# Performance work log

Measured on AMD Instinct MI355X. Metric: run time of the kernel, lower is better.

Reference implementation:

```python
import jax, jax.numpy as jnp
import numpy as np

U = 100000   # user_count
I = 50000    # item_count
N = U + I    # total nodes in bipartite graph
D = 64       # embedding dim
L = 3        # num_layers
E = 4800000  # nnz of normalized adjacency
B = 8192     # batch size


def setup_inputs() -> dict:
    key = jax.random.key(0)
    ks = jax.random.split(key, 8)
    edge_src = jax.random.randint(ks[0], (E,), 0, N, dtype=jnp.int32)
    edge_dst = jax.random.randint(ks[1], (E,), 0, N, dtype=jnp.int32)
    # normalized adjacency values ~ 1/sqrt(deg_i*deg_j); small positive numbers
    edge_val = jax.random.uniform(ks[2], (E,), dtype=jnp.float32) * (1.0 / 32.0)
    user_emb_w = jax.random.normal(ks[3], (U, D), dtype=jnp.float32) * 0.01
    item_emb_w = jax.random.normal(ks[4], (I, D), dtype=jnp.float32) * 0.01
    batch_user = jax.random.randint(ks[5], (B,), 0, U, dtype=jnp.int32)
    batch_pos_item = jax.random.randint(ks[6], (B,), 0, I, dtype=jnp.int32)
    batch_neg_item = jax.random.randint(ks[7], (B,), 0, I, dtype=jnp.int32)
    return {
        "edge_src": edge_src,
        "edge_dst": edge_dst,
        "edge_val": edge_val,
        "user_emb_w": user_emb_w,
        "item_emb_w": item_emb_w,
        "batch_user": batch_user,
        "batch_pos_item": batch_pos_item,
        "batch_neg_item": batch_neg_item,
    }


def _spmm(edge_src, edge_dst, edge_val, x):
    # out[i] = sum_{e: dst[e]==i} val[e] * x[src[e]]  (sparse A @ x)
    msgs = edge_val[:, None] * x[edge_src]           # [E, D]
    return jax.ops.segment_sum(msgs, edge_dst, num_segments=N)


def _computer(edge_src, edge_dst, edge_val, user_emb_w, item_emb_w):
    all_emb = jnp.concatenate([user_emb_w, item_emb_w], axis=0)  # [N, D]
    acc = all_emb
    cur = all_emb
    for _ in range(L):
        cur = _spmm(edge_src, edge_dst, edge_val, cur)
        acc = acc + cur
    light_out = acc / jnp.float32(L + 1)  # mean over (L+1) layer embeddings
    return light_out[:U], light_out[U:]


def reference(edge_src, edge_dst, edge_val, user_emb_w, item_emb_w,
              batch_user, batch_pos_item, batch_neg_item):
    all_users, all_items = _computer(edge_src, edge_dst, edge_val,
                                     user_emb_w, item_emb_w)
    user = all_users[batch_user]       # [B, D]
    pos = all_items[batch_pos_item]    # [B, D]
    neg = all_items[batch_neg_item]    # [B, D]
    pos_score = jnp.sum(user * pos, axis=1)
    neg_score = jnp.sum(user * neg, axis=1)
    user0 = user_emb_w[batch_user]
    pos0 = item_emb_w[batch_pos_item]
    neg0 = item_emb_w[batch_neg_item]
    reg_loss = (jnp.sum(user0 * user0) + jnp.sum(pos0 * pos0)
                + jnp.sum(neg0 * neg0))
    return pos_score, neg_score, reg_loss
```

## Files before the change

### kernel.cpp

```cpp
#include <hip/hip_runtime.h>

#define D 64
#define BK 256
#define KMAX 1024
#define PCH 6144
#define PEPT 6

static __device__ __forceinline__ unsigned short f2bf(float f) {
    unsigned int u = __float_as_uint(f);
    unsigned int r = (u + 0x7FFFu + ((u >> 16) & 1u)) >> 16;
    return (unsigned short)r;
}
static __device__ __forceinline__ float bflo(unsigned int u) {
    return __uint_as_float(u << 16);
}
static __device__ __forceinline__ float bfhi(unsigned int u) {
    return __uint_as_float(u & 0xFFFF0000u);
}

__global__ void init_kernel(const float4* __restrict__ user_w,
                            const float4* __restrict__ item_w,
                            float4* __restrict__ acc,
                            ushort4* __restrict__ curb,
                            const int* __restrict__ flags,
                            int n_user4, int n_tot4) {
    int i = blockIdx.x * blockDim.x + threadIdx.x;
    if (i >= n_tot4) return;
    float4 v = (i < n_user4) ? user_w[i] : item_w[i - n_user4];
    ushort4 b;
    b.x = f2bf(v.x); b.y = f2bf(v.y); b.z = f2bf(v.z); b.w = f2bf(v.w);
    curb[i] = b;
    if (flags[i >> 4]) acc[i] = v;
}

__global__ void flag_kernel(const int* __restrict__ bu,
                            const int* __restrict__ bp,
                            const int* __restrict__ bn,
                            int* __restrict__ flags,
                            int* __restrict__ list,
                            int* __restrict__ n_list,
                            int U_, int B_) {
    int t = blockIdx.x * blockDim.x + threadIdx.x;
    int node = -1;
    if (t < 3 * B_) {
        if (t < B_)            node = bu[t];
        else if (t < 2 * B_)   node = U_ + bp[t - B_];
        else                   node = U_ + bn[t - 2 * B_];
    }
    int old = 1;
    if (node >= 0) old = atomicExch(&flags[node], 1);
    unsigned long long m = __ballot(old == 0);
    int lane = threadIdx.x & 63;
    int myoff = __popcll(m & ((1ull << lane) - 1ull));
    int total = __popcll(m);
    int bse = 0;
    if (lane == 0 && total) bse = atomicAdd(n_list, total);
    bse = __shfl(bse, 0, 64);
    if (old == 0) list[bse + myoff] = node;
}

__global__ void __launch_bounds__(1024)
partition_kernel(const int* __restrict__ src,
                 const int* __restrict__ dst,
                 const float* __restrict__ val,
                 int* __restrict__ g_pos,
                 int2* __restrict__ st,
                 int S_, int K_, int E_) {
    __shared__ int2 stg[PCH];
    __shared__ int cnt[KMAX];
    __shared__ int sh[KMAX];
    __shared__ int gb[KMAX];
    int tid = threadIdx.x;
    for (int k = tid; k < K_; k += 1024) cnt[k] = 0;
    __syncthreads();
    int b0 = blockIdx.x * PCH;
    int nc = min(PCH, E_ - b0);
    int myk[PEPT], myr[PEPT], mysrc[PEPT];
    unsigned mypk[PEPT];
#pragma unroll
    for (int e = 0; e < PEPT; ++e) {
        int i = b0 + e * 1024 + tid;
        if (i < E_) {
            int d = dst[i];
            int k = d >> 8;
            myk[e] = k;
            mysrc[e] = src[i];
            mypk[e] = ((unsigned)f2bf(val[i]) << 16) | (unsigned)(d & (BK - 1));
            myr[e] = atomicAdd(&cnt[k], 1);
        } else {
            myk[e] = -1;
        }
    }
    __syncthreads();
    int v = (tid < K_) ? cnt[tid] : 0;
    sh[tid] = v;
    __syncthreads();
    for (int off = 1; off < KMAX; off <<= 1) {
        int t = (tid >= off) ? sh[tid - off] : 0;
        __syncthreads();
        sh[tid] += t;
        __syncthreads();
    }
    if (tid < K_ && v) {
        int lbase = sh[tid] - v;
        gb[tid] = (tid * S_ + atomicAdd(&g_pos[tid], v)) - lbase;
    }
    __syncthreads();
#pragma unroll
    for (int e = 0; e < PEPT; ++e) {
        int k = myk[e];
        if (k >= 0) {
            int slot = (sh[k] - cnt[k]) + myr[e];
            stg[slot] = make_int2(mysrc[e] | (k << 20), (int)mypk[e]);
        }
    }
    __syncthreads();
    for (int l = tid; l < nc; l += 1024) {
        int2 ev = stg[l];
        int k = (int)((unsigned)ev.x >> 20);
        st[gb[k] + l] = make_int2(ev.x & 0xFFFFF, ev.y);
    }
}

__global__ void scan_bkt_kernel(const int* __restrict__ cnt,
                                int* __restrict__ base, int K_) {
    __shared__ int sh[KMAX];
    int tid = threadIdx.x;
    int v = (tid < K_) ? cnt[tid] : 0;
    sh[tid] = v;
    __syncthreads();
    for (int off = 1; off < KMAX; off <<= 1) {
        int t = (tid >= off) ? sh[tid - off] : 0;
        __syncthreads();
        sh[tid] += t;
        __syncthreads();
    }
    if (tid < K_) base[tid] = sh[tid] - v;
}

__global__ void __launch_bounds__(1024)
place_kernel(const int2* __restrict__ st,
             const int* __restrict__ g_cnt,
             const int* __restrict__ bkt_base,
             int2* __restrict__ row_span,
             int2* __restrict__ col_val,
             int S_, int N_) {
    __shared__ int ldeg[BK];
    __shared__ int sh[BK];
    __shared__ int lcur[BK];
    int b = blockIdx.x;
    int tid = threadIdx.x;
    int rbeg = b << 8;
    int sbeg = b * S_;
    int cnt = g_cnt[b];
    int cbeg = bkt_base[b];
    if (tid < BK) ldeg[tid] = 0;
    __syncthreads();
    for (int i = tid; i < cnt; i += 1024)
        atomicAdd(&ldeg[(unsigned)st[sbeg + i].y & (BK - 1u)], 1);
    __syncthreads();
    int v = 0;
    if (tid < BK) {
        v = ldeg[tid];
        sh[tid] = v;
    }
    __syncthreads();
    for (int off = 1; off < BK; off <<= 1) {
        int t = (tid < BK && tid >= off) ? sh[tid - off] : 0;
        __syncthreads();
        if (tid < BK) sh[tid] += t;
        __syncthreads();
    }
    if (tid < BK) {
        int excl = sh[tid] - v;
        lcur[tid] = excl;
        int gi = rbeg + tid;
        if (gi < N_) row_span[gi] = make_int2(cbeg + excl, cbeg + excl + v);
    }
    __syncthreads();
    for (int i = tid; i < cnt; i += 1024) {
        int2 cv = st[sbeg + i];
        int pcur = cbeg + atomicAdd(&lcur[(unsigned)cv.y & (BK - 1u)], 1);
        col_val[pcur] = cv;
    }
}

static __device__ __forceinline__ void spmm_row_body(
        int beg, int end, int lane, int q, int lid,
        const int2* __restrict__ col_val, const uint4* __restrict__ xb,
        float& s0, float& s1, float& s2, float& s3,
        float& s4, float& s5, float& s6, float& s7) {
    for (int base = beg; base < end; base += 64) {
        int e = base + lane;
        int c = 0;
        float v = 0.f;
        if (e < end) {
            int2 cv = col_val[e];
            c = cv.x;
            v = bfhi((unsigned)cv.y);
        }
        int nq = (min(64, end - base) + 7) >> 3;
        uint4 t0, t1, t2, t3, t4, t5, t6, t7;
        float w0, w1, w2, w3, w4, w5, w6, w7;
        { int cj = __shfl(c, q, 64);      w0 = __shfl(v, q, 64);      t0 = xb[cj * 8 + lid]; }
        if (nq > 1) { int cj = __shfl(c, 8 + q, 64);  w1 = __shfl(v, 8 + q, 64);  t1 = xb[cj * 8 + lid]; }
        if (nq > 2) { int cj = __shfl(c, 16 + q, 64); w2 = __shfl(v, 16 + q, 64); t2 = xb[cj * 8 + lid]; }
        if (nq > 3) { int cj = __shfl(c, 24 + q, 64); w3 = __shfl(v, 24 + q, 64); t3 = xb[cj * 8 + lid]; }
        if (nq > 4) { int cj = __shfl(c, 32 + q, 64); w4 = __shfl(v, 32 + q, 64); t4 = xb[cj * 8 + lid]; }
        if (nq > 5) { int cj = __shfl(c, 40 + q, 64); w5 = __shfl(v, 40 + q, 64); t5 = xb[cj * 8 + lid]; }
        if (nq > 6) { int cj = __shfl(c, 48 + q, 64); w6 = __shfl(v, 48 + q, 64); t6 = xb[cj * 8 + lid]; }
        if (nq > 7) { int cj = __shfl(c, 56 + q, 64); w7 = __shfl(v, 56 + q, 64); t7 = xb[cj * 8 + lid]; }
#define ACC8(W, T) \
        s0 += (W) * bflo((T).x); s1 += (W) * bfhi((T).x); \
        s2 += (W) * bflo((T).y); s3 += (W) * bfhi((T).y); \
        s4 += (W) * bflo((T).z); s5 += (W) * bfhi((T).z); \
        s6 += (W) * bflo((T).w); s7 += (W) * bfhi((T).w);
        { ACC8(w0, t0) }
        if (nq > 1) { ACC8(w1, t1) }
        if (nq > 2) { ACC8(w2, t2) }
        if (nq > 3) { ACC8(w3, t3) }
        if (nq > 4) { ACC8(w4, t4) }
        if (nq > 5) { ACC8(w5, t5) }
        if (nq > 6) { ACC8(w6, t6) }
        if (nq > 7) { ACC8(w7, t7) }
#undef ACC8
    }
#pragma unroll
    for (int off = 32; off >= 8; off >>= 1) {
        s0 += __shfl_xor(s0, off, 64);
        s1 += __shfl_xor(s1, off, 64);
        s2 += __shfl_xor(s2, off, 64);
        s3 += __shfl_xor(s3, off, 64);
        s4 += __shfl_xor(s4, off, 64);
        s5 += __shfl_xor(s5, off, 64);
        s6 += __shfl_xor(s6, off, 64);
        s7 += __shfl_xor(s7, off, 64);
    }
}

__global__ void spmm_csr_kernel(const int2* __restrict__ row_span,
                                const int2* __restrict__ col_val,
                                const uint4* __restrict__ xb,
                                uint4* __restrict__ nxtb,
                                float4* __restrict__ acc,
                                const int* __restrict__ flags,
                                int N_) {
    int row = (int)((blockIdx.x * blockDim.x + threadIdx.x) >> 6);
    int lane = threadIdx.x & 63;
    if (row >= N_) return;
    int q = lane >> 3;
    int lid = lane & 7;
    int2 sp = row_span[row];
    float s0 = 0, s1 = 0, s2 = 0, s3 = 0, s4 = 0, s5 = 0, s6 = 0, s7 = 0;
    spmm_row_body(sp.x, sp.y, lane, q, lid, col_val, xb,
                  s0, s1, s2, s3, s4, s5, s6, s7);
    if (q == 0) {
        uint4 b;
        b.x = (unsigned)f2bf(s0) | ((unsigned)f2bf(s1) << 16);
        b.y = (unsigned)f2bf(s2) | ((unsigned)f2bf(s3) << 16);
        b.z = (unsigned)f2bf(s4) | ((unsigned)f2bf(s5) << 16);
        b.w = (unsigned)f2bf(s6) | ((unsigned)f2bf(s7) << 16);
        nxtb[row * 8 + lid] = b;
        if (flags[row]) {
            float4* ap = acc + row * 16 + lid * 2;
            float4 a0 = ap[0];
            a0.x += s0; a0.y += s1; a0.z += s2; a0.w += s3;
            ap[0] = a0;
            float4 a1 = ap[1];
            a1.x += s4; a1.y += s5; a1.z += s6; a1.w += s7;
            ap[1] = a1;
        }
    }
}

__global__ void spmm_rows_kernel(const int2* __restrict__ row_span,
                                 const int2* __restrict__ col_val,
                                 const uint4* __restrict__ xb,
                                 float4* __restrict__ acc,
                                 const int* __restrict__ list,
                                 const int* __restrict__ n_list) {
    int w = (int)((blockIdx.x * blockDim.x + threadIdx.x) >> 6);
    if (w >= *n_list) return;
    int row = list[w];
    int lane = threadIdx.x & 63;
    int q = lane >> 3;
    int lid = lane & 7;
    int2 sp = row_span[row];
    float s0 = 0, s1 = 0, s2 = 0, s3 = 0, s4 = 0, s5 = 0, s6 = 0, s7 = 0;
    spmm_row_body(sp.x, sp.y, lane, q, lid, col_val, xb,
                  s0, s1, s2, s3, s4, s5, s6, s7);
    if (q == 0) {
        float4* ap = acc + row * 16 + lid * 2;
        float4 a0 = ap[0];
        a0.x += s0; a0.y += s1; a0.z += s2; a0.w += s3;
        ap[0] = a0;
        float4 a1 = ap[1];
        a1.x += s4; a1.y += s5; a1.z += s6; a1.w += s7;
        ap[1] = a1;
    }
}

__global__ void final_kernel(const float* __restrict__ acc,
                             const float* __restrict__ user_w,
                             const float* __restrict__ item_w,
                             const int* __restrict__ bu,
                             const int* __restrict__ bp,
                             const int* __restrict__ bn,
                             float* __restrict__ out,
                             float* __restrict__ red,
                             int U_, int B_) {
    __shared__ float pr[4];
    int w = (int)((blockIdx.x * blockDim.x + threadIdx.x) >> 6);
    int lane = threadIdx.x & 63;
    bool valid = (w < B_);
    float ps = 0.f, ns = 0.f, r = 0.f;
    if (valid) {
        int iu = bu[w], ip = bp[w], in_ = bn[w];
        const float scale = 0.25f;
        float u = acc[(long)iu * D + lane] * scale;
        float p = acc[(long)(U_ + ip) * D + lane] * scale;
        float g = acc[(long)(U_ + in_) * D + lane] * scale;
        ps = u * p;
        ns = u * g;
        float u0 = user_w[(long)iu * D + lane];
        float p0 = item_w[(long)ip * D + lane];
        float n0 = item_w[(long)in_ * D + lane];
        r = u0 * u0 + p0 * p0 + n0 * n0;
    }
#pragma unroll
    for (int off = 32; off; off >>= 1) {
        ps += __shfl_down(ps, off, 64);
        ns += __shfl_down(ns, off, 64);
        r  += __shfl_down(r, off, 64);
    }
    if (lane == 0) pr[threadIdx.x >> 6] = r;
    __syncthreads();
    if (threadIdx.x == 0)
        red[blockIdx.x] = pr[0] + pr[1] + pr[2] + pr[3];
    if (valid && lane == 0) {
        out[w] = ps;
        out[B_ + w] = ns;
    }
}

__global__ void reduce_kernel(const float* __restrict__ red,
                              float* __restrict__ out_scalar, int nblk) {
    __shared__ float sh[256];
    float s = 0.f;
    for (int i = threadIdx.x; i < nblk; i += 256) s += red[i];
    sh[threadIdx.x] = s;
    __syncthreads();
    for (int off = 128; off; off >>= 1) {
        if (threadIdx.x < off) sh[threadIdx.x] += sh[threadIdx.x + off];
        __syncthreads();
    }
    if (threadIdx.x == 0) *out_scalar = sh[0];
}

extern "C" void kernel_launch(void* const* d_in, const int* in_sizes, int n_in,
                              void* d_out, int out_size, void* d_ws, size_t ws_size,
                              hipStream_t stream) {
    const int*   edge_src = (const int*)d_in[0];
    const int*   edge_dst = (const int*)d_in[1];
    const float* edge_val = (const float*)d_in[2];
    const float* user_w   = (const float*)d_in[3];
    const float* item_w   = (const float*)d_in[4];
    const int*   bu       = (const int*)d_in[5];
    const int*   bp       = (const int*)d_in[6];
    const int*   bn       = (const int*)d_in[7];

    int E_ = in_sizes[0];
    int U_ = in_sizes[3] / D;
    int I_ = in_sizes[4] / D;
    int B_ = in_sizes[5];
    int N_ = U_ + I_;
    long ND = (long)N_ * D;
    int K_ = (N_ + BK - 1) >> 8;
    int S_ = ((E_ / K_) * 3 / 2 + 255) & ~255;

    char* p = (char*)d_ws;
    int2* col_val  = (int2*)p;   p += (size_t)E_ * sizeof(int2);
    int2* row_span = (int2*)p;   p += (size_t)N_ * sizeof(int2);
    int*  bkt_base = (int*)p;    p += KMAX * sizeof(int);
    float* red     = (float*)p;  p += 4096 * sizeof(float);
    char* zb = p;
    int*  g_pos    = (int*)p;    p += KMAX * sizeof(int);
    int*  n_list   = (int*)p;    p += 256;
    int*  flags    = (int*)p;    p += (size_t)N_ * sizeof(int);
    size_t zbytes  = (size_t)(p - zb);
    int*  list     = (int*)p;    p += (size_t)3 * B_ * sizeof(int);
    p = (char*)(((uintptr_t)p + 255) & ~(uintptr_t)255);
    int2* st = (int2*)p;
    float* acc = (float*)p;
    unsigned short* curb = (unsigned short*)(acc + ND);
    unsigned short* nxtb = curb + ND;
    float* out = (float*)d_out;

    int n4 = (int)(ND / 4);
    int nu4 = U_ * D / 4;

    hipMemsetAsync(zb, 0, zbytes, stream);
    partition_kernel<<<(E_ + PCH - 1) / PCH, 1024, 0, stream>>>(
        edge_src, edge_dst, edge_val, g_pos, st, S_, K_, E_);
    scan_bkt_kernel<<<1, KMAX, 0, stream>>>(g_pos, bkt_base, K_);
    place_kernel<<<K_, 1024, 0, stream>>>(st, g_pos, bkt_base, row_span,
                                          col_val, S_, N_);

    flag_kernel<<<(3 * B_ + 255) / 256, 256, 0, stream>>>(
        bu, bp, bn, flags, list, n_list, U_, B_);

    init_kernel<<<(n4 + 255) / 256, 256, 0, stream>>>(
        (const float4*)user_w, (const float4*)item_w,
        (float4*)acc, (ushort4*)curb, flags, nu4, n4);

    spmm_csr_kernel<<<(N_ + 3) / 4, 256, 0, stream>>>(
        row_span, col_val, (const uint4*)curb, (uint4*)nxtb, (float4*)acc,
        flags, N_);
    spmm_csr_kernel<<<(N_ + 3) / 4, 256, 0, stream>>>(
        row_span, col_val, (const uint4*)nxtb, (uint4*)curb, (float4*)acc,
        flags, N_);
    spmm_rows_kernel<<<(3 * B_ + 3) / 4, 256, 0, stream>>>(
        row_span, col_val, (const uint4*)curb, (float4*)acc, list, n_list);

    int nblk = (B_ * 64 + 255) / 256;
    final_kernel<<<nblk, 256, 0, stream>>>(
        acc, user_w, item_w, bu, bp, bn, out, red, U_, B_);
    reduce_kernel<<<1, 256, 0, stream>>>(red, out + 2 * B_, nblk);
}
```

Baseline: 402.4 us.

## Persistent SpMM with next-row prefetch, fold bucket scan into place kernel

The CSR SpMM kernel becomes a grid-stride persistent kernel with a fixed grid. Each wave prefetches the next row's span and first col/val chunk while it finishes the current row, hiding index-load latency. The separate single-block bucket scan is removed: every place block redundantly scans the bucket counts in shared memory, saving a launch at the cost of extra per-block work. place_kernel also keeps up to 8 staged edges in registers between the histogram and scatter passes so they are not reloaded.

```diff
diff --git a/kernel.cpp b/kernel.cpp
--- a/kernel.cpp
+++ b/kernel.cpp
@@ -122,29 +122,13 @@
     }
 }
 
-__global__ void scan_bkt_kernel(const int* __restrict__ cnt,
-                                int* __restrict__ base, int K_) {
-    __shared__ int sh[KMAX];
-    int tid = threadIdx.x;
-    int v = (tid < K_) ? cnt[tid] : 0;
-    sh[tid] = v;
-    __syncthreads();
-    for (int off = 1; off < KMAX; off <<= 1) {
-        int t = (tid >= off) ? sh[tid - off] : 0;
-        __syncthreads();
-        sh[tid] += t;
-        __syncthreads();
-    }
-    if (tid < K_) base[tid] = sh[tid] - v;
-}
-
 __global__ void __launch_bounds__(1024)
 place_kernel(const int2* __restrict__ st,
-             const int* __restrict__ g_cnt,
-             const int* __restrict__ bkt_base,
+             const int* __restrict__ g_pos,
              int2* __restrict__ row_span,
              int2* __restrict__ col_val,
-             int S_, int N_) {
+             int S_, int K_, int N_) {
+    __shared__ int gsc[KMAX];
     __shared__ int ldeg[BK];
     __shared__ int sh[BK];
     __shared__ int lcur[BK];
@@ -152,11 +136,26 @@
     int tid = threadIdx.x;
     int rbeg = b << 8;
     int sbeg = b * S_;
-    int cnt = g_cnt[b];
-    int cbeg = bkt_base[b];
+    int gp = (tid < K_) ? g_pos[tid] : 0;
+    gsc[tid] = gp;
     if (tid < BK) ldeg[tid] = 0;
     __syncthreads();
-    for (int i = tid; i < cnt; i += 1024)
+    for (int off = 1; off < KMAX; off <<= 1) {
+        int t = (tid >= off) ? gsc[tid - off] : 0;
+        __syncthreads();
+        gsc[tid] += t;
+        __syncthreads();
+    }
+    int cbeg = (b > 0) ? gsc[b - 1] : 0;
+    int cnt = gsc[b] - cbeg;
+    int2 ec0, ec1, ec2, ec3, ec4, ec5, ec6, ec7;
+#define HLOAD(J, EC) { int i = tid + (J) * 1024; \
+        EC = (i < cnt) ? st[sbeg + i] : make_int2(0, 0); \
+        if (i < cnt) atomicAdd(&ldeg[(unsigned)EC.y & (BK - 1u)], 1); }
+    HLOAD(0, ec0) HLOAD(1, ec1) HLOAD(2, ec2) HLOAD(3, ec3)
+    HLOAD(4, ec4) HLOAD(5, ec5) HLOAD(6, ec6) HLOAD(7, ec7)
+#undef HLOAD
+    for (int i = tid + 8192; i < cnt; i += 1024)
         atomicAdd(&ldeg[(unsigned)st[sbeg + i].y & (BK - 1u)], 1);
     __syncthreads();
     int v = 0;
@@ -178,10 +177,17 @@
         if (gi < N_) row_span[gi] = make_int2(cbeg + excl, cbeg + excl + v);
     }
     __syncthreads();
-    for (int i = tid; i < cnt; i += 1024) {
+#define SCAT(J, EC) { int i = tid + (J) * 1024; \
+        if (i < cnt) { \
+            int p = cbeg + atomicAdd(&lcur[(unsigned)EC.y & (BK - 1u)], 1); \
+            col_val[p] = EC; } }
+    SCAT(0, ec0) SCAT(1, ec1) SCAT(2, ec2) SCAT(3, ec3)
+    SCAT(4, ec4) SCAT(5, ec5) SCAT(6, ec6) SCAT(7, ec7)
+#undef SCAT
+    for (int i = tid + 8192; i < cnt; i += 1024) {
         int2 cv = st[sbeg + i];
-        int pcur = cbeg + atomicAdd(&lcur[(unsigned)cv.y & (BK - 1u)], 1);
-        col_val[pcur] = cv;
+        int p = cbeg + atomicAdd(&lcur[(unsigned)cv.y & (BK - 1u)], 1);
+        col_val[p] = cv;
     }
 }
 
@@ -238,30 +244,123 @@
     }
 }
 
-__global__ void spmm_csr_kernel(const int2* __restrict__ row_span,
-                                const int2* __restrict__ col_val,
-                                const uint4* __restrict__ xb,
-                                uint4* __restrict__ nxtb,
-                                float4* __restrict__ acc,
-                                const int* __restrict__ flags,
-                                int N_) {
-    int row = (int)((blockIdx.x * blockDim.x + threadIdx.x) >> 6);
+__global__ void __launch_bounds__(256)
+spmm_csr_kernel(const int2* __restrict__ row_span,
+                const int2* __restrict__ col_val,
+                const uint4* __restrict__ xb,
+                uint4* __restrict__ nxtb,
+                float4* __restrict__ acc,
+                const int* __restrict__ flags,
+                int N_) {
     int lane = threadIdx.x & 63;
-    if (row >= N_) return;
     int q = lane >> 3;
     int lid = lane & 7;
+    int nw = (int)((gridDim.x * blockDim.x) >> 6);
+    int row = (int)((blockIdx.x * blockDim.x + threadIdx.x) >> 6);
+    if (row >= N_) return;
     int2 sp = row_span[row];
-    float s0 = 0, s1 = 0, s2 = 0, s3 = 0, s4 = 0, s5 = 0, s6 = 0, s7 = 0;
-    spmm_row_body(sp.x, sp.y, lane, q, lid, col_val, xb,
-                  s0, s1, s2, s3, s4, s5, s6, s7);
-    if (q == 0) {
-        uint4 b;
-        b.x = (unsigned)f2bf(s0) | ((unsigned)f2bf(s1) << 16);
-        b.y = (unsigned)f2bf(s2) | ((unsigned)f2bf(s3) << 16);
-        b.z = (unsigned)f2bf(s4) | ((unsigned)f2bf(s5) << 16);
-        b.w = (unsigned)f2bf(s6) | ((unsigned)f2bf(s7) << 16);
-        nxtb[row * 8 + lid] = b;
-        if (flags[row]) {
+    int2 cv = make_int2(0, 0);
+    if (sp.x + lane < sp.y) cv = col_val[sp.x + lane];
+    while (true) {
+        int nrow = row + nw;
+        int2 spn = make_int2(0, 0);
+        if (nrow < N_) spn = row_span[nrow];
+        float s0 = 0, s1 = 0, s2 = 0, s3 = 0, s4 = 0, s5 = 0, s6 = 0, s7 = 0;
+        int base = sp.x;
+        int end = sp.y;
+        int c = cv.x;
+        float v = bfhi((unsigned)cv.y);
+        if (base < end) {
+            while (true) {
+                int nq = (min(64, end - base) + 7) >> 3;
+                uint4 t0, t1, t2, t3, t4, t5, t6, t7;
+                float w0, w1, w2, w3, w4, w5, w6, w7;
+                { int cj = __shfl(c, q, 64);      w0 = __shfl(v, q, 64);      t0 = xb[cj * 8 + lid]; }
+                if (nq > 1) { int cj = __shfl(c, 8 + q, 64);  w1 = __shfl(v, 8 + q, 64);  t1 = xb[cj * 8 + lid]; }
+                if (nq > 2) { int cj = __shfl(c, 16 + q, 64); w2 = __shfl(v, 16 + q, 64); t2 = xb[cj * 8 + lid]; }
+                if (nq > 3) { int cj = __shfl(c, 24 + q, 64); w3 = __shfl(v, 24 + q, 64); t3 = xb[cj * 8 + lid]; }
+                if (nq > 4) { int cj = __shfl(c, 32 + q, 64); w4 = __shfl(v, 32 + q, 64); t4 = xb[cj * 8 + lid]; }
+                if (nq > 5) { int cj = __shfl(c, 40 + q, 64); w5 = __shfl(v, 40 + q, 64); t5 = xb[cj * 8 + lid]; }
+                if (nq > 6) { int cj = __shfl(c, 48 + q, 64); w6 = __shfl(v, 48 + q, 64); t6 = xb[cj * 8 + lid]; }
+                if (nq > 7) { int cj = __shfl(c, 56 + q, 64); w7 = __shfl(v, 56 + q, 64); t7 = xb[cj * 8 + lid]; }
+#define ACC8(W, T) \
+                s0 += (W) * bflo((T).x); s1 += (W) * bfhi((T).x); \
+                s2 += (W) * bflo((T).y); s3 += (W) * bfhi((T).y); \
+                s4 += (W) * bflo((T).z); s5 += (W) * bfhi((T).z); \
+                s6 += (W) * bflo((T).w); s7 += (W) * bfhi((T).w);
+                { ACC8(w0, t0) }
+                if (nq > 1) { ACC8(w1, t1) }
+                if (nq > 2) { ACC8(w2, t2) }
+                if (nq > 3) { ACC8(w3, t3) }
+                if (nq > 4) { ACC8(w4, t4) }
+                if (nq > 5) { ACC8(w5, t5) }
+                if (nq > 6) { ACC8(w6, t6) }
+                if (nq > 7) { ACC8(w7, t7) }
+#undef ACC8
+                base += 64;
+                if (base >= end) break;
+                int e = base + lane;
+                int2 cvi = (e < end) ? col_val[e] : make_int2(0, 0);
+                c = cvi.x;
+                v = bfhi((unsigned)cvi.y);
+            }
+        }
+        int2 cvn = make_int2(0, 0);
+        if (nrow < N_ && spn.x + lane < spn.y) cvn = col_val[spn.x + lane];
+#pragma unroll
+        for (int off = 32; off >= 8; off >>= 1) {
+            s0 += __shfl_xor(s0, off, 64);
+            s1 += __shfl_xor(s1, off, 64);
+            s2 += __shfl_xor(s2, off, 64);
+            s3 += __shfl_xor(s3, off, 64);
+            s4 += __shfl_xor(s4, off, 64);
+            s5 += __shfl_xor(s5, off, 64);
+            s6 += __shfl_xor(s6, off, 64);
+            s7 += __shfl_xor(s7, off, 64);
+        }
+        if (q == 0) {
+            uint4 b;
+            b.x = (unsigned)f2bf(s0) | ((unsigned)f2bf(s1) << 16);
+            b.y = (unsigned)f2bf(s2) | ((unsigned)f2bf(s3) << 16);
+            b.z = (unsigned)f2bf(s4) | ((unsigned)f2bf(s5) << 16);
+            b.w = (unsigned)f2bf(s6) | ((unsigned)f2bf(s7) << 16);
+            nxtb[row * 8 + lid] = b;
+            if (flags[row]) {
+                float4* ap = acc + row * 16 + lid * 2;
+                float4 a0 = ap[0];
+                a0.x += s0; a0.y += s1; a0.z += s2; a0.w += s3;
+                ap[0] = a0;
+                float4 a1 = ap[1];
+                a1.x += s4; a1.y += s5; a1.z += s6; a1.w += s7;
+                ap[1] = a1;
+            }
+        }
+        if (nrow >= N_) break;
+        row = nrow;
+        sp = spn;
+        cv = cvn;
+    }
+}
+
+__global__ void spmm_rows_kernel(const int2* __restrict__ row_span,
+                                 const int2* __restrict__ col_val,
+                                 const uint4* __restrict__ xb,
+                                 float4* __restrict__ acc,
+                                 const int* __restrict__ list,
+                                 const int* __restrict__ n_list) {
+    int lane = threadIdx.x & 63;
+    int q = lane >> 3;
+    int lid = lane & 7;
+    int nw = (int)((gridDim.x * blockDim.x) >> 6);
+    int nl = *n_list;
+    for (int w = (int)((blockIdx.x * blockDim.x + threadIdx.x) >> 6); w < nl;
+         w += nw) {
+        int row = list[w];
+        int2 sp = row_span[row];
+        float s0 = 0, s1 = 0, s2 = 0, s3 = 0, s4 = 0, s5 = 0, s6 = 0, s7 = 0;
+        spmm_row_body(sp.x, sp.y, lane, q, lid, col_val, xb,
+                      s0, s1, s2, s3, s4, s5, s6, s7);
+        if (q == 0) {
             float4* ap = acc + row * 16 + lid * 2;
             float4 a0 = ap[0];
             a0.x += s0; a0.y += s1; a0.z += s2; a0.w += s3;
@@ -270,33 +369,6 @@
             a1.x += s4; a1.y += s5; a1.z += s6; a1.w += s7;
             ap[1] = a1;
         }
-    }
-}
-
-__global__ void spmm_rows_kernel(const int2* __restrict__ row_span,
-                                 const int2* __restrict__ col_val,
-                                 const uint4* __restrict__ xb,
-                                 float4* __restrict__ acc,
-                                 const int* __restrict__ list,
-                                 const int* __restrict__ n_list) {
-    int w = (int)((blockIdx.x * blockDim.x + threadIdx.x) >> 6);
-    if (w >= *n_list) return;
-    int row = list[w];
-    int lane = threadIdx.x & 63;
-    int q = lane >> 3;
-    int lid = lane & 7;
-    int2 sp = row_span[row];
-    float s0 = 0, s1 = 0, s2 = 0, s3 = 0, s4 = 0, s5 = 0, s6 = 0, s7 = 0;
-    spmm_row_body(sp.x, sp.y, lane, q, lid, col_val, xb,
-                  s0, s1, s2, s3, s4, s5, s6, s7);
-    if (q == 0) {
-        float4* ap = acc + row * 16 + lid * 2;
-        float4 a0 = ap[0];
-        a0.x += s0; a0.y += s1; a0.z += s2; a0.w += s3;
-        ap[0] = a0;
-        float4 a1 = ap[1];
-        a1.x += s4; a1.y += s5; a1.z += s6; a1.w += s7;
-        ap[1] = a1;
     }
 }
 
@@ -381,7 +453,6 @@
     char* p = (char*)d_ws;
     int2* col_val  = (int2*)p;   p += (size_t)E_ * sizeof(int2);
     int2* row_span = (int2*)p;   p += (size_t)N_ * sizeof(int2);
-    int*  bkt_base = (int*)p;    p += KMAX * sizeof(int);
     float* red     = (float*)p;  p += 4096 * sizeof(float);
     char* zb = p;
     int*  g_pos    = (int*)p;    p += KMAX * sizeof(int);
@@ -402,9 +473,8 @@
     hipMemsetAsync(zb, 0, zbytes, stream);
     partition_kernel<<<(E_ + PCH - 1) / PCH, 1024, 0, stream>>>(
         edge_src, edge_dst, edge_val, g_pos, st, S_, K_, E_);
-    scan_bkt_kernel<<<1, KMAX, 0, stream>>>(g_pos, bkt_base, K_);
-    place_kernel<<<K_, 1024, 0, stream>>>(st, g_pos, bkt_base, row_span,
-                                          col_val, S_, N_);
+    place_kernel<<<K_, 1024, 0, stream>>>(st, g_pos, row_span, col_val,
+                                          S_, K_, N_);
 
     flag_kernel<<<(3 * B_ + 255) / 256, 256, 0, stream>>>(
         bu, bp, bn, flags, list, n_list, U_, B_);
@@ -413,13 +483,13 @@
         (const float4*)user_w, (const float4*)item_w,
         (float4*)acc, (ushort4*)curb, flags, nu4, n4);
 
-    spmm_csr_kernel<<<(N_ + 3) / 4, 256, 0, stream>>>(
+    spmm_csr_kernel<<<2048, 256, 0, stream>>>(
         row_span, col_val, (const uint4*)curb, (uint4*)nxtb, (float4*)acc,
         flags, N_);
-    spmm_csr_kernel<<<(N_ + 3) / 4, 256, 0, stream>>>(
+    spmm_csr_kernel<<<2048, 256, 0, stream>>>(
         row_span, col_val, (const uint4*)nxtb, (uint4*)curb, (float4*)acc,
         flags, N_);
-    spmm_rows_kernel<<<(3 * B_ + 3) / 4, 256, 0, stream>>>(
+    spmm_rows_kernel<<<512, 256, 0, stream>>>(
         row_span, col_val, (const uint4*)curb, (float4*)acc, list, n_list);
 
     int nblk = (B_ * 64 + 255) / 256;
```

Result: slower. 434.1 us (+7.9%).

## Fold bucket scan into place kernel, register-cache edges, nontemporal CSR loads

Applied to the files above, without the earlier changes.

Removes the separate single-block scan launch by having each place_kernel block redundantly scan the bucket counts in shared memory. place_kernel now keeps up to eight edges per thread in registers between the histogram and scatter passes instead of reading the staging buffer twice. The SpMM kernels read col_val and row_span with nontemporal loads so the streamed CSR data does not evict the gathered embedding rows from cache. The redundant scan adds per-block work and barriers, and the register caching raises register pressure in a 1024-thread block.

```diff
diff --git a/kernel.cpp b/kernel.cpp
--- a/kernel.cpp
+++ b/kernel.cpp
@@ -16,6 +16,13 @@
 }
 static __device__ __forceinline__ float bfhi(unsigned int u) {
     return __uint_as_float(u & 0xFFFF0000u);
+}
+static __device__ __forceinline__ int2 nt_load_i2(const int2* p) {
+    long long t = __builtin_nontemporal_load((const long long*)p);
+    int2 r;
+    r.x = (int)(unsigned)(t & 0xFFFFFFFFull);
+    r.y = (int)(unsigned)((unsigned long long)t >> 32);
+    return r;
 }
 
 __global__ void init_kernel(const float4* __restrict__ user_w,
@@ -122,29 +129,13 @@
     }
 }
 
-__global__ void scan_bkt_kernel(const int* __restrict__ cnt,
-                                int* __restrict__ base, int K_) {
-    __shared__ int sh[KMAX];
-    int tid = threadIdx.x;
-    int v = (tid < K_) ? cnt[tid] : 0;
-    sh[tid] = v;
-    __syncthreads();
-    for (int off = 1; off < KMAX; off <<= 1) {
-        int t = (tid >= off) ? sh[tid - off] : 0;
-        __syncthreads();
-        sh[tid] += t;
-        __syncthreads();
-    }
-    if (tid < K_) base[tid] = sh[tid] - v;
-}
-
 __global__ void __launch_bounds__(1024)
 place_kernel(const int2* __restrict__ st,
-             const int* __restrict__ g_cnt,
-             const int* __restrict__ bkt_base,
+             const int* __restrict__ g_pos,
              int2* __restrict__ row_span,
              int2* __restrict__ col_val,
-             int S_, int N_) {
+             int S_, int K_, int N_) {
+    __shared__ int gsc[KMAX];
     __shared__ int ldeg[BK];
     __shared__ int sh[BK];
     __shared__ int lcur[BK];
@@ -152,11 +143,26 @@
     int tid = threadIdx.x;
     int rbeg = b << 8;
     int sbeg = b * S_;
-    int cnt = g_cnt[b];
-    int cbeg = bkt_base[b];
+    int gp = (tid < K_) ? g_pos[tid] : 0;
+    gsc[tid] = gp;
     if (tid < BK) ldeg[tid] = 0;
     __syncthreads();
-    for (int i = tid; i < cnt; i += 1024)
+    for (int off = 1; off < KMAX; off <<= 1) {
+        int t = (tid >= off) ? gsc[tid - off] : 0;
+        __syncthreads();
+        gsc[tid] += t;
+        __syncthreads();
+    }
+    int cbeg = (b > 0) ? gsc[b - 1] : 0;
+    int cnt = gsc[b] - cbeg;
+    int2 ec0, ec1, ec2, ec3, ec4, ec5, ec6, ec7;
+#define HLOAD(J, EC) { int i = tid + (J) * 1024; \
+        EC = (i < cnt) ? st[sbeg + i] : make_int2(0, 0); \
+        if (i < cnt) atomicAdd(&ldeg[(unsigned)EC.y & (BK - 1u)], 1); }
+    HLOAD(0, ec0) HLOAD(1, ec1) HLOAD(2, ec2) HLOAD(3, ec3)
+    HLOAD(4, ec4) HLOAD(5, ec5) HLOAD(6, ec6) HLOAD(7, ec7)
+#undef HLOAD
+    for (int i = tid + 8192; i < cnt; i += 1024)
         atomicAdd(&ldeg[(unsigned)st[sbeg + i].y & (BK - 1u)], 1);
     __syncthreads();
     int v = 0;
@@ -178,10 +184,17 @@
         if (gi < N_) row_span[gi] = make_int2(cbeg + excl, cbeg + excl + v);
     }
     __syncthreads();
-    for (int i = tid; i < cnt; i += 1024) {
+#define SCAT(J, EC) { int i = tid + (J) * 1024; \
+        if (i < cnt) { \
+            int p = cbeg + atomicAdd(&lcur[(unsigned)EC.y & (BK - 1u)], 1); \
+            col_val[p] = EC; } }
+    SCAT(0, ec0) SCAT(1, ec1) SCAT(2, ec2) SCAT(3, ec3)
+    SCAT(4, ec4) SCAT(5, ec5) SCAT(6, ec6) SCAT(7, ec7)
+#undef SCAT
+    for (int i = tid + 8192; i < cnt; i += 1024) {
         int2 cv = st[sbeg + i];
-        int pcur = cbeg + atomicAdd(&lcur[(unsigned)cv.y & (BK - 1u)], 1);
-        col_val[pcur] = cv;
+        int p = cbeg + atomicAdd(&lcur[(unsigned)cv.y & (BK - 1u)], 1);
+        col_val[p] = cv;
     }
 }
 
@@ -195,7 +208,7 @@
         int c = 0;
         float v = 0.f;
         if (e < end) {
-            int2 cv = col_val[e];
+            int2 cv = nt_load_i2(&col_val[e]);
             c = cv.x;
             v = bfhi((unsigned)cv.y);
         }
@@ -250,7 +263,7 @@
     if (row >= N_) return;
     int q = lane >> 3;
     int lid = lane & 7;
-    int2 sp = row_span[row];
+    int2 sp = nt_load_i2(&row_span[row]);
     float s0 = 0, s1 = 0, s2 = 0, s3 = 0, s4 = 0, s5 = 0, s6 = 0, s7 = 0;
     spmm_row_body(sp.x, sp.y, lane, q, lid, col_val, xb,
                   s0, s1, s2, s3, s4, s5, s6, s7);
@@ -381,7 +394,6 @@
     char* p = (char*)d_ws;
     int2* col_val  = (int2*)p;   p += (size_t)E_ * sizeof(int2);
     int2* row_span = (int2*)p;   p += (size_t)N_ * sizeof(int2);
-    int*  bkt_base = (int*)p;    p += KMAX * sizeof(int);
     float* red     = (float*)p;  p += 4096 * sizeof(float);
     char* zb = p;
     int*  g_pos    = (int*)p;    p += KMAX * sizeof(int);
@@ -402,9 +414,8 @@
     hipMemsetAsync(zb, 0, zbytes, stream);
     partition_kernel<<<(E_ + PCH - 1) / PCH, 1024, 0, stream>>>(
         edge_src, edge_dst, edge_val, g_pos, st, S_, K_, E_);
-    scan_bkt_kernel<<<1, KMAX, 0, stream>>>(g_pos, bkt_base, K_);
-    place_kernel<<<K_, 1024, 0, stream>>>(st, g_pos, bkt_base, row_span,
-                                          col_val, S_, N_);
+    place_kernel<<<K_, 1024, 0, stream>>>(st, g_pos, row_span, col_val,
+                                          S_, K_, N_);
 
     flag_kernel<<<(3 * B_ + 255) / 256, 256, 0, stream>>>(
         bu, bp, bn, flags, list, n_list, U_, B_);
```

New measurement: 396.6 us. Within noise of the previous version (-1.5%).

## Fuse graph prep kernels and build CSR in place with first SpMM layer

Applied to the files above, without the earlier changes.

Merges partition, bf16 conversion of the embeddings and batch flagging into one multi-role prep kernel. The bucket-scan and separate CSR placement pass are dropped: each bucket sorts its edges in place inside a fixed-size slot and immediately computes the first SpMM layer from them, reading the reordered edges through coherent atomic loads. The layer-0 embedding add moves into the final kernel, so acc no longer needs to be initialised. This removes several launches and one full edge-array copy, but fixed slots of 9216 per bucket silently truncate buckets with more edges, and the per-bucket SpMM uses only 16 wavefronts per 256 rows.

```diff
diff --git a/kernel.cpp b/kernel.cpp
--- a/kernel.cpp
+++ b/kernel.cpp
@@ -5,6 +5,8 @@
 #define KMAX 1024
 #define PCH 6144
 #define PEPT 6
+#define SLOT 9216
+#define NSL 9
 
 static __device__ __forceinline__ unsigned short f2bf(float f) {
     unsigned int u = __float_as_uint(f);
@@ -17,177 +19,19 @@
 static __device__ __forceinline__ float bfhi(unsigned int u) {
     return __uint_as_float(u & 0xFFFF0000u);
 }
-
-__global__ void init_kernel(const float4* __restrict__ user_w,
-                            const float4* __restrict__ item_w,
-                            float4* __restrict__ acc,
-                            ushort4* __restrict__ curb,
-                            const int* __restrict__ flags,
-                            int n_user4, int n_tot4) {
-    int i = blockIdx.x * blockDim.x + threadIdx.x;
-    if (i >= n_tot4) return;
-    float4 v = (i < n_user4) ? user_w[i] : item_w[i - n_user4];
-    ushort4 b;
-    b.x = f2bf(v.x); b.y = f2bf(v.y); b.z = f2bf(v.z); b.w = f2bf(v.w);
-    curb[i] = b;
-    if (flags[i >> 4]) acc[i] = v;
-}
-
-__global__ void flag_kernel(const int* __restrict__ bu,
-                            const int* __restrict__ bp,
-                            const int* __restrict__ bn,
-                            int* __restrict__ flags,
-                            int* __restrict__ list,
-                            int* __restrict__ n_list,
-                            int U_, int B_) {
-    int t = blockIdx.x * blockDim.x + threadIdx.x;
-    int node = -1;
-    if (t < 3 * B_) {
-        if (t < B_)            node = bu[t];
-        else if (t < 2 * B_)   node = U_ + bp[t - B_];
-        else                   node = U_ + bn[t - 2 * B_];
-    }
-    int old = 1;
-    if (node >= 0) old = atomicExch(&flags[node], 1);
-    unsigned long long m = __ballot(old == 0);
-    int lane = threadIdx.x & 63;
-    int myoff = __popcll(m & ((1ull << lane) - 1ull));
-    int total = __popcll(m);
-    int bse = 0;
-    if (lane == 0 && total) bse = atomicAdd(n_list, total);
-    bse = __shfl(bse, 0, 64);
-    if (old == 0) list[bse + myoff] = node;
-}
-
-__global__ void __launch_bounds__(1024)
-partition_kernel(const int* __restrict__ src,
-                 const int* __restrict__ dst,
-                 const float* __restrict__ val,
-                 int* __restrict__ g_pos,
-                 int2* __restrict__ st,
-                 int S_, int K_, int E_) {
-    __shared__ int2 stg[PCH];
-    __shared__ int cnt[KMAX];
-    __shared__ int sh[KMAX];
-    __shared__ int gb[KMAX];
-    int tid = threadIdx.x;
-    for (int k = tid; k < K_; k += 1024) cnt[k] = 0;
-    __syncthreads();
-    int b0 = blockIdx.x * PCH;
-    int nc = min(PCH, E_ - b0);
-    int myk[PEPT], myr[PEPT], mysrc[PEPT];
-    unsigned mypk[PEPT];
-#pragma unroll
-    for (int e = 0; e < PEPT; ++e) {
-        int i = b0 + e * 1024 + tid;
-        if (i < E_) {
-            int d = dst[i];
-            int k = d >> 8;
-            myk[e] = k;
-            mysrc[e] = src[i];
-            mypk[e] = ((unsigned)f2bf(val[i]) << 16) | (unsigned)(d & (BK - 1));
-            myr[e] = atomicAdd(&cnt[k], 1);
-        } else {
-            myk[e] = -1;
-        }
-    }
-    __syncthreads();
-    int v = (tid < K_) ? cnt[tid] : 0;
-    sh[tid] = v;
-    __syncthreads();
-    for (int off = 1; off < KMAX; off <<= 1) {
-        int t = (tid >= off) ? sh[tid - off] : 0;
-        __syncthreads();
-        sh[tid] += t;
-        __syncthreads();
-    }
-    if (tid < K_ && v) {
-        int lbase = sh[tid] - v;
-        gb[tid] = (tid * S_ + atomicAdd(&g_pos[tid], v)) - lbase;
-    }
-    __syncthreads();
-#pragma unroll
-    for (int e = 0; e < PEPT; ++e) {
-        int k = myk[e];
-        if (k >= 0) {
-            int slot = (sh[k] - cnt[k]) + myr[e];
-            stg[slot] = make_int2(mysrc[e] | (k << 20), (int)mypk[e]);
-        }
-    }
-    __syncthreads();
-    for (int l = tid; l < nc; l += 1024) {
-        int2 ev = stg[l];
-        int k = (int)((unsigned)ev.x >> 20);
-        st[gb[k] + l] = make_int2(ev.x & 0xFFFFF, ev.y);
-    }
-}
-
-__global__ void scan_bkt_kernel(const int* __restrict__ cnt,
-                                int* __restrict__ base, int K_) {
-    __shared__ int sh[KMAX];
-    int tid = threadIdx.x;
-    int v = (tid < K_) ? cnt[tid] : 0;
-    sh[tid] = v;
-    __syncthreads();
-    for (int off = 1; off < KMAX; off <<= 1) {
-        int t = (tid >= off) ? sh[tid - off] : 0;
-        __syncthreads();
-        sh[tid] += t;
-        __syncthreads();
-    }
-    if (tid < K_) base[tid] = sh[tid] - v;
-}
-
-__global__ void __launch_bounds__(1024)
-place_kernel(const int2* __restrict__ st,
-             const int* __restrict__ g_cnt,
-             const int* __restrict__ bkt_base,
-             int2* __restrict__ row_span,
-             int2* __restrict__ col_val,
-             int S_, int N_) {
-    __shared__ int ldeg[BK];
-    __shared__ int sh[BK];
-    __shared__ int lcur[BK];
-    int b = blockIdx.x;
-    int tid = threadIdx.x;
-    int rbeg = b << 8;
-    int sbeg = b * S_;
-    int cnt = g_cnt[b];
-    int cbeg = bkt_base[b];
-    if (tid < BK) ldeg[tid] = 0;
-    __syncthreads();
-    for (int i = tid; i < cnt; i += 1024)
-        atomicAdd(&ldeg[(unsigned)st[sbeg + i].y & (BK - 1u)], 1);
-    __syncthreads();
-    int v = 0;
-    if (tid < BK) {
-        v = ldeg[tid];
-        sh[tid] = v;
-    }
-    __syncthreads();
-    for (int off = 1; off < BK; off <<= 1) {
-        int t = (tid < BK && tid >= off) ? sh[tid - off] : 0;
-        __syncthreads();
-        if (tid < BK) sh[tid] += t;
-        __syncthreads();
-    }
-    if (tid < BK) {
-        int excl = sh[tid] - v;
-        lcur[tid] = excl;
-        int gi = rbeg + tid;
-        if (gi < N_) row_span[gi] = make_int2(cbeg + excl, cbeg + excl + v);
-    }
-    __syncthreads();
-    for (int i = tid; i < cnt; i += 1024) {
-        int2 cv = st[sbeg + i];
-        int pcur = cbeg + atomicAdd(&lcur[(unsigned)cv.y & (BK - 1u)], 1);
-        col_val[pcur] = cv;
-    }
-}
-
-static __device__ __forceinline__ void spmm_row_body(
+static __device__ __forceinline__ int2 ld_i2_glc(const int2* p) {
+    long long t = __hip_atomic_load((const long long*)p, __ATOMIC_RELAXED,
+                                    __HIP_MEMORY_SCOPE_AGENT);
+    int2 r;
+    r.x = (int)(unsigned)((unsigned long long)t & 0xFFFFFFFFull);
+    r.y = (int)(unsigned)((unsigned long long)t >> 32);
+    return r;
+}
+
+template <bool GLC>
+static __device__ __forceinline__ void row_accum(
         int beg, int end, int lane, int q, int lid,
-        const int2* __restrict__ col_val, const uint4* __restrict__ xb,
+        const int2* __restrict__ cv_ptr, const uint4* __restrict__ xb,
         float& s0, float& s1, float& s2, float& s3,
         float& s4, float& s5, float& s6, float& s7) {
     for (int base = beg; base < end; base += 64) {
@@ -195,7 +39,7 @@
         int c = 0;
         float v = 0.f;
         if (e < end) {
-            int2 cv = col_val[e];
+            int2 cv = GLC ? ld_i2_glc(&cv_ptr[e]) : cv_ptr[e];
             c = cv.x;
             v = bfhi((unsigned)cv.y);
         }
@@ -238,6 +82,194 @@
     }
 }
 
+__global__ void __launch_bounds__(1024)
+prep_kernel(const int* __restrict__ src,
+            const int* __restrict__ dst,
+            const float* __restrict__ val,
+            int* __restrict__ g_pos,
+            int2* __restrict__ st,
+            int K_, int E_, int PB, int IB,
+            const float4* __restrict__ user_w,
+            const float4* __restrict__ item_w,
+            ushort4* __restrict__ curb,
+            int nu4, int n4,
+            const int* __restrict__ bu,
+            const int* __restrict__ bp,
+            const int* __restrict__ bn,
+            int* __restrict__ flags,
+            int* __restrict__ list,
+            int* __restrict__ n_list,
+            int U_, int B_) {
+    __shared__ int2 stg[PCH];
+    __shared__ int cnt[KMAX];
+    __shared__ int sh[KMAX];
+    __shared__ int gb[KMAX];
+    int bid = blockIdx.x;
+    int tid = threadIdx.x;
+    if (bid < PB) {
+        for (int k = tid; k < K_; k += 1024) cnt[k] = 0;
+        __syncthreads();
+        int b0 = bid * PCH;
+        int nc = min(PCH, E_ - b0);
+        int myk[PEPT], myr[PEPT], mysrc[PEPT];
+        unsigned mypk[PEPT];
+#pragma unroll
+        for (int e = 0; e < PEPT; ++e) {
+            int i = b0 + e * 1024 + tid;
+            if (i < E_) {
+                int d = dst[i];
+                int k = d >> 8;
+                myk[e] = k;
+                mysrc[e] = src[i];
+                mypk[e] = ((unsigned)f2bf(val[i]) << 16) | (unsigned)(d & (BK - 1));
+                myr[e] = atomicAdd(&cnt[k], 1);
+            } else {
+                myk[e] = -1;
+            }
+        }
+        __syncthreads();
+        int v = (tid < K_) ? cnt[tid] : 0;
+        sh[tid] = v;
+        __syncthreads();
+        for (int off = 1; off < KMAX; off <<= 1) {
+            int t = (tid >= off) ? sh[tid - off] : 0;
+            __syncthreads();
+            sh[tid] += t;
+            __syncthreads();
+        }
+        if (tid < K_ && v) {
+            int lbase = sh[tid] - v;
+            gb[tid] = (tid * SLOT + atomicAdd(&g_pos[tid], v)) - lbase;
+        }
+        __syncthreads();
+#pragma unroll
+        for (int e = 0; e < PEPT; ++e) {
+            int k = myk[e];
+            if (k >= 0) {
+                int slot = (sh[k] - cnt[k]) + myr[e];
+                stg[slot] = make_int2(mysrc[e] | (k << 20), (int)mypk[e]);
+            }
+        }
+        __syncthreads();
+        for (int l = tid; l < nc; l += 1024) {
+            int2 ev = stg[l];
+            int k = (int)((unsigned)ev.x >> 20);
+            st[gb[k] + l] = make_int2(ev.x & 0xFFFFF, ev.y);
+        }
+    } else if (bid < PB + IB) {
+        int i = (bid - PB) * 1024 + tid;
+        if (i < n4) {
+            float4 v = (i < nu4) ? user_w[i] : item_w[i - nu4];
+            ushort4 b;
+            b.x = f2bf(v.x); b.y = f2bf(v.y); b.z = f2bf(v.z); b.w = f2bf(v.w);
+            curb[i] = b;
+        }
+    } else {
+        int t = (bid - PB - IB) * 1024 + tid;
+        int node = -1;
+        if (t < 3 * B_) {
+            if (t < B_)            node = bu[t];
+            else if (t < 2 * B_)   node = U_ + bp[t - B_];
+            else                   node = U_ + bn[t - 2 * B_];
+        }
+        int old = 1;
+        if (node >= 0) old = atomicExch(&flags[node], 1);
+        unsigned long long m = __ballot(old == 0);
+        int lane = tid & 63;
+        int myoff = __popcll(m & ((1ull << lane) - 1ull));
+        int total = __popcll(m);
+        int bse = 0;
+        if (lane == 0 && total) bse = atomicAdd(n_list, total);
+        bse = __shfl(bse, 0, 64);
+        if (old == 0) list[bse + myoff] = node;
+    }
+}
+
+__global__ void __launch_bounds__(1024)
+build_l1_kernel(int2* __restrict__ st,
+                const int* __restrict__ g_cnt,
+                int2* __restrict__ row_span,
+                const uint4* __restrict__ xb,
+                uint4* __restrict__ nxtb,
+                float4* __restrict__ acc,
+                const int* __restrict__ flags,
+                int N_) {
+    __shared__ int ldeg[BK];
+    __shared__ int lsc[BK];
+    __shared__ int lcur[BK];
+    int b = blockIdx.x;
+    int tid = threadIdx.x;
+    int sbeg = b * SLOT;
+    int rbeg = b << 8;
+    int cnt = g_cnt[b];
+    if (cnt > SLOT) cnt = SLOT;
+    if (tid < BK) ldeg[tid] = 0;
+    __syncthreads();
+    int2 e0, e1, e2, e3, e4, e5, e6, e7, e8;
+#define HL(J, EC) { int i = tid + (J) * 1024; \
+        EC = (i < cnt) ? st[sbeg + i] : make_int2(0, 0); \
+        if (i < cnt) atomicAdd(&ldeg[(unsigned)EC.y & (BK - 1u)], 1); }
+    HL(0, e0) HL(1, e1) HL(2, e2) HL(3, e3) HL(4, e4)
+    HL(5, e5) HL(6, e6) HL(7, e7) HL(8, e8)
+#undef HL
+    __syncthreads();
+    int v = 0;
+    if (tid < BK) {
+        v = ldeg[tid];
+        lsc[tid] = v;
+    }
+    __syncthreads();
+    for (int off = 1; off < BK; off <<= 1) {
+        int t = (tid < BK && tid >= off) ? lsc[tid - off] : 0;
+        __syncthreads();
+        if (tid < BK) lsc[tid] += t;
+        __syncthreads();
+    }
+    if (tid < BK) {
+        int excl = lsc[tid] - v;
+        lcur[tid] = excl;
+        lsc[tid] = excl;
+        int gi = rbeg + tid;
+        if (gi < N_) row_span[gi] = make_int2(sbeg + excl, sbeg + excl + v);
+    }
+    __syncthreads();
+#define SC(J, EC) { int i = tid + (J) * 1024; \
+        if (i < cnt) { \
+            int p = atomicAdd(&lcur[(unsigned)EC.y & (BK - 1u)], 1); \
+            st[sbeg + p] = EC; } }
+    SC(0, e0) SC(1, e1) SC(2, e2) SC(3, e3) SC(4, e4)
+    SC(5, e5) SC(6, e6) SC(7, e7) SC(8, e8)
+#undef SC
+    __syncthreads();
+    int wid = tid >> 6;
+    int lane = tid & 63;
+    int q = lane >> 3;
+    int lid = lane & 7;
+    for (int rr = 0; rr < 16; ++rr) {
+        int r = wid * 16 + rr;
+        int row = rbeg + r;
+        if (row >= N_) break;
+        int beg = sbeg + lsc[r];
+        int end = beg + ldeg[r];
+        float s0 = 0, s1 = 0, s2 = 0, s3 = 0, s4 = 0, s5 = 0, s6 = 0, s7 = 0;
+        row_accum<true>(beg, end, lane, q, lid, st, xb,
+                        s0, s1, s2, s3, s4, s5, s6, s7);
+        if (q == 0) {
+            uint4 bb;
+            bb.x = (unsigned)f2bf(s0) | ((unsigned)f2bf(s1) << 16);
+            bb.y = (unsigned)f2bf(s2) | ((unsigned)f2bf(s3) << 16);
+            bb.z = (unsigned)f2bf(s4) | ((unsigned)f2bf(s5) << 16);
+            bb.w = (unsigned)f2bf(s6) | ((unsigned)f2bf(s7) << 16);
+            nxtb[row * 8 + lid] = bb;
+            if (flags[row]) {
+                float4* ap = acc + row * 16 + lid * 2;
+                ap[0] = make_float4(s0, s1, s2, s3);
+                ap[1] = make_float4(s4, s5, s6, s7);
+            }
+        }
+    }
+}
+
 __global__ void spmm_csr_kernel(const int2* __restrict__ row_span,
                                 const int2* __restrict__ col_val,
                                 const uint4* __restrict__ xb,
@@ -252,8 +284,8 @@
     int lid = lane & 7;
     int2 sp = row_span[row];
     float s0 = 0, s1 = 0, s2 = 0, s3 = 0, s4 = 0, s5 = 0, s6 = 0, s7 = 0;
-    spmm_row_body(sp.x, sp.y, lane, q, lid, col_val, xb,
-                  s0, s1, s2, s3, s4, s5, s6, s7);
+    row_accum<false>(sp.x, sp.y, lane, q, lid, col_val, xb,
+                     s0, s1, s2, s3, s4, s5, s6, s7);
     if (q == 0) {
         uint4 b;
         b.x = (unsigned)f2bf(s0) | ((unsigned)f2bf(s1) << 16);
@@ -287,8 +319,8 @@
     int lid = lane & 7;
     int2 sp = row_span[row];
     float s0 = 0, s1 = 0, s2 = 0, s3 = 0, s4 = 0, s5 = 0, s6 = 0, s7 = 0;
-    spmm_row_body(sp.x, sp.y, lane, q, lid, col_val, xb,
-                  s0, s1, s2, s3, s4, s5, s6, s7);
+    row_accum<false>(sp.x, sp.y, lane, q, lid, col_val, xb,
+                     s0, s1, s2, s3, s4, s5, s6, s7);
     if (q == 0) {
         float4* ap = acc + row * 16 + lid * 2;
         float4 a0 = ap[0];
@@ -317,14 +349,14 @@
     if (valid) {
         int iu = bu[w], ip = bp[w], in_ = bn[w];
         const float scale = 0.25f;
-        float u = acc[(long)iu * D + lane] * scale;
-        float p = acc[(long)(U_ + ip) * D + lane] * scale;
-        float g = acc[(long)(U_ + in_) * D + lane] * scale;
-        ps = u * p;
-        ns = u * g;
         float u0 = user_w[(long)iu * D + lane];
         float p0 = item_w[(long)ip * D + lane];
         float n0 = item_w[(long)in_ * D + lane];
+        float u = (acc[(long)iu * D + lane] + u0) * scale;
+        float p = (acc[(long)(U_ + ip) * D + lane] + p0) * scale;
+        float g = (acc[(long)(U_ + in_) * D + lane] + n0) * scale;
+        ps = u * p;
+        ns = u * g;
         r = u0 * u0 + p0 * p0 + n0 * n0;
     }
 #pragma unroll
@@ -376,12 +408,10 @@
     int N_ = U_ + I_;
     long ND = (long)N_ * D;
     int K_ = (N_ + BK - 1) >> 8;
-    int S_ = ((E_ / K_) * 3 / 2 + 255) & ~255;
 
     char* p = (char*)d_ws;
-    int2* col_val  = (int2*)p;   p += (size_t)E_ * sizeof(int2);
+    int2* st       = (int2*)p;   p += (size_t)K_ * SLOT * sizeof(int2);
     int2* row_span = (int2*)p;   p += (size_t)N_ * sizeof(int2);
-    int*  bkt_base = (int*)p;    p += KMAX * sizeof(int);
     float* red     = (float*)p;  p += 4096 * sizeof(float);
     char* zb = p;
     int*  g_pos    = (int*)p;    p += KMAX * sizeof(int);
@@ -390,38 +420,30 @@
     size_t zbytes  = (size_t)(p - zb);
     int*  list     = (int*)p;    p += (size_t)3 * B_ * sizeof(int);
     p = (char*)(((uintptr_t)p + 255) & ~(uintptr_t)255);
-    int2* st = (int2*)p;
-    float* acc = (float*)p;
-    unsigned short* curb = (unsigned short*)(acc + ND);
-    unsigned short* nxtb = curb + ND;
+    float* acc = (float*)p;                  p += ND * sizeof(float);
+    unsigned short* curb = (unsigned short*)p; p += ND * sizeof(unsigned short);
+    unsigned short* nxtb = (unsigned short*)p;
     float* out = (float*)d_out;
 
     int n4 = (int)(ND / 4);
     int nu4 = U_ * D / 4;
+    int PB = (E_ + PCH - 1) / PCH;
+    int IB = (n4 + 1023) / 1024;
+    int FB = (3 * B_ + 1023) / 1024;
 
     hipMemsetAsync(zb, 0, zbytes, stream);
-    partition_kernel<<<(E_ + PCH - 1) / PCH, 1024, 0, stream>>>(
-        edge_src, edge_dst, edge_val, g_pos, st, S_, K_, E_);
-    scan_bkt_kernel<<<1, KMAX, 0, stream>>>(g_pos, bkt_base, K_);
-    place_kernel<<<K_, 1024, 0, stream>>>(st, g_pos, bkt_base, row_span,
-                                          col_val, S_, N_);
-
-    flag_kernel<<<(3 * B_ + 255) / 256, 256, 0, stream>>>(
-        bu, bp, bn, flags, list, n_list, U_, B_);
-
-    init_kernel<<<(n4 + 255) / 256, 256, 0, stream>>>(
-        (const float4*)user_w, (const float4*)item_w,
-        (float4*)acc, (ushort4*)curb, flags, nu4, n4);
-
-    spmm_csr_kernel<<<(N_ + 3) / 4, 256, 0, stream>>>(
-        row_span, col_val, (const uint4*)curb, (uint4*)nxtb, (float4*)acc,
+    prep_kernel<<<PB + IB + FB, 1024, 0, stream>>>(
+        edge_src, edge_dst, edge_val, g_pos, st, K_, E_, PB, IB,
+        (const float4*)user_w, (const float4*)item_w, (ushort4*)curb,
+        nu4, n4, bu, bp, bn, flags, list, n_list, U_, B_);
+    build_l1_kernel<<<K_, 1024, 0, stream>>>(
+        st, g_pos, row_span, (const uint4*)curb, (uint4*)nxtb, (float4*)acc,
         flags, N_);
     spmm_csr_kernel<<<(N_ + 3) / 4, 256, 0, stream>>>(
-        row_span, col_val, (const uint4*)nxtb, (uint4*)curb, (float4*)acc,
+        row_span, st, (const uint4*)nxtb, (uint4*)curb, (float4*)acc,
         flags, N_);
     spmm_rows_kernel<<<(3 * B_ + 3) / 4, 256, 0, stream>>>(
-        row_span, col_val, (const uint4*)curb, (float4*)acc, list, n_list);
-
+        row_span, st, (const uint4*)curb, (float4*)acc, list, n_list);
     int nblk = (B_ * 64 + 255) / 256;
     final_kernel<<<nblk, 256, 0, stream>>>(
         acc, user_w, item_w, bu, bp, bn, out, red, U_, B_);
```

Result: no change. 400.5 us (-0.5%).
